# Optimization experiments

Hardware: AMD Instinct MI355X
Metric: run time of the kernel (lower is better)

## Reference

```python
import jax, jax.numpy as jnp
import numpy as np

N_SRC0, N_DST0 = 200000, 50000
N_DST1 = 10000
D_IN, D_HID = 128, 128


def _sage_mean(h, src, dst, n_dst, W_self, b_self, W_neigh, b_neigh, act):
    # gather messages from src nodes, mean-aggregate per dst node
    msg = h[src]                                             # [E, D]
    agg = jax.ops.segment_sum(msg, dst, num_segments=n_dst)  # [n_dst, D]
    deg = jax.ops.segment_sum(jnp.ones(dst.shape, h.dtype), dst, num_segments=n_dst)
    h_neigh = agg / jnp.maximum(deg, 1.0)[:, None]
    # DGL block convention: dst nodes are the first n_dst src nodes
    rst = h[:n_dst] @ W_self + b_self + h_neigh @ W_neigh + b_neigh
    return jax.nn.relu(rst) if act else rst


def setup_inputs() -> dict:
    key = jax.random.key(0)
    ks = jax.random.split(key, 12)
    s = 1.0 / np.sqrt(D_HID)
    return {
        "features": jax.random.normal(ks[0], (N_SRC0, D_IN), jnp.float32),
        "src0": jax.random.randint(ks[1], (800000,), 0, N_SRC0),
        "dst0": jax.random.randint(ks[2], (800000,), 0, N_DST0),
        "src1": jax.random.randint(ks[3], (160000,), 0, N_DST0),
        "dst1": jax.random.randint(ks[4], (160000,), 0, N_DST1),
        "W_init": jax.random.uniform(ks[5], (D_IN, D_HID), jnp.float32, -s, s),
        "b_init": jax.random.uniform(ks[6], (D_HID,), jnp.float32, -s, s),
        "W_self": jax.random.uniform(ks[7], (D_HID, D_HID), jnp.float32, -s, s),
        "b_self": jax.random.uniform(ks[8], (D_HID,), jnp.float32, -s, s),
        "W_neigh": jax.random.uniform(ks[9], (D_HID, D_HID), jnp.float32, -s, s),
        "b_neigh": jax.random.uniform(ks[10], (D_HID,), jnp.float32, -s, s),
    }


def reference(features, src0, dst0, src1, dst1, W_init, b_init, W_self, b_self, W_neigh, b_neigh):
    # fc_init + activation
    h = jax.nn.relu(features @ W_init + b_init)              # [N_SRC0, D_HID]
    # block 0 (act_flag True), dropout p=0.0 is identity
    h = _sage_mean(h, src0, dst0, N_DST0, W_self, b_self, W_neigh, b_neigh, act=True)
    # block 1 (last block: act_flag False)
    h = _sage_mean(h, src1, dst1, N_DST1, W_self, b_self, W_neigh, b_neigh, act=False)
    return jnp.squeeze(h, axis=1) if h.shape[1] == 1 else h  # h.squeeze(1) no-op for D_HID>1
```

## Files before the change

### kernel.cpp

```cpp
#include <hip/hip_runtime.h>
#include <stdint.h>
#include <stddef.h>


#define DIM 128
constexpr int N_SRC0 = 200000;
constexpr int N_DST0 = 50000;
constexpr int N_DST1 = 10000;
constexpr int E0 = 800000;
constexpr int E1 = 160000;
constexpr int MAXDEG = 64;

typedef __attribute__((ext_vector_type(8))) short bf16x8;
typedef __attribute__((ext_vector_type(4))) float f32x4;

__device__ __forceinline__ uint16_t f2bf(float f) {
  union { float f; uint32_t u; } v; v.f = f;
  return (uint16_t)((v.u + 0x7FFFu + ((v.u >> 16) & 1u)) >> 16);
}
__device__ __forceinline__ float bf2f(uint16_t h) {
  union { uint32_t u; float f; } v; v.u = ((uint32_t)h) << 16;
  return v.f;
}

__global__ __launch_bounds__(512) void prep_w_kernel(
    const float* __restrict__ W0, const float* __restrict__ W1,
    const float* __restrict__ W2, uint16_t* __restrict__ Wf,
    int* __restrict__ cnt, int ncnt) {
  int gid = blockIdx.x * 512 + threadIdx.x;
  if (gid < 3 * 16384) {
    int m = gid >> 14, idx = gid & 16383;
    const float* W = m == 0 ? W0 : (m == 1 ? W1 : W2);
    int j = idx & 7, lane = (idx >> 3) & 63, nt = (idx >> 9) & 7, kc = idx >> 12;
    int k = kc * 32 + (lane >> 4) * 8 + j;
    int n = nt * 16 + (lane & 15);
    Wf[gid] = f2bf(W[k * DIM + n]);
  }
  int z = gid - 3 * 16384;
  if (z >= 0 && z < ncnt) cnt[z] = 0;
}

__global__ __launch_bounds__(256) void place_kernel(
    const int* __restrict__ src0, const int* __restrict__ dst0,
    const int* __restrict__ src1, const int* __restrict__ dst1,
    int* __restrict__ cnt0, int* __restrict__ cnt1,
    int* __restrict__ eslot0, int* __restrict__ eslot1) {
  int part = blockIdx.x & 7;
  int bpp  = gridDim.x >> 3;
  int bidx = blockIdx.x >> 3;
  const int4* s04 = (const int4*)src0;
  const int4* d04 = (const int4*)dst0;
  const int4* s14 = (const int4*)src1;
  const int4* d14 = (const int4*)dst1;

  int lo = part * (N_DST0 / 8), hi = lo + (N_DST0 / 8);
  for (int i = bidx * 256 + threadIdx.x; i < E0 / 4; i += bpp * 256) {
    int4 d = d04[i]; int4 s = s04[i];
    if (d.x >= lo && d.x < hi) { int p = atomicAdd(&cnt0[d.x], 1); if (p < MAXDEG) eslot0[(size_t)d.x * MAXDEG + p] = s.x; }
    if (d.y >= lo && d.y < hi) { int p = atomicAdd(&cnt0[d.y], 1); if (p < MAXDEG) eslot0[(size_t)d.y * MAXDEG + p] = s.y; }
    if (d.z >= lo && d.z < hi) { int p = atomicAdd(&cnt0[d.z], 1); if (p < MAXDEG) eslot0[(size_t)d.z * MAXDEG + p] = s.z; }
    if (d.w >= lo && d.w < hi) { int p = atomicAdd(&cnt0[d.w], 1); if (p < MAXDEG) eslot0[(size_t)d.w * MAXDEG + p] = s.w; }
  }
  int lo1 = part * (N_DST1 / 8), hi1 = lo1 + (N_DST1 / 8);
  for (int i = bidx * 256 + threadIdx.x; i < E1 / 4; i += bpp * 256) {
    int4 d = d14[i]; int4 s = s14[i];
    if (d.x >= lo1 && d.x < hi1) { int p = atomicAdd(&cnt1[d.x], 1); if (p < MAXDEG) eslot1[(size_t)d.x * MAXDEG + p] = s.x; }
    if (d.y >= lo1 && d.y < hi1) { int p = atomicAdd(&cnt1[d.y], 1); if (p < MAXDEG) eslot1[(size_t)d.y * MAXDEG + p] = s.y; }
    if (d.z >= lo1 && d.z < hi1) { int p = atomicAdd(&cnt1[d.z], 1); if (p < MAXDEG) eslot1[(size_t)d.z * MAXDEG + p] = s.z; }
    if (d.w >= lo1 && d.w < hi1) { int p = atomicAdd(&cnt1[d.w], 1); if (p < MAXDEG) eslot1[(size_t)d.w * MAXDEG + p] = s.w; }
  }
}

__global__ __launch_bounds__(256) void fc_init_kernel(
    const float* __restrict__ feat, const uint16_t* __restrict__ Wf,
    const float* __restrict__ bias, uint16_t* __restrict__ hout) {
  __shared__ uint16_t wl[16384];
  __shared__ __align__(16) float tile[2][4096];
  {
    const uint4* g = (const uint4*)Wf;
    uint4* s = (uint4*)wl;
    for (int i = threadIdx.x; i < 2048; i += 256) s[i] = g[i];
  }
  const int tid = threadIdx.x;
  const int w = tid >> 6, lane = tid & 63;
  const int q = lane >> 4, m16 = lane & 15;
  const int sl = w >> 1, nh = w & 1;

  float bv[4];
#pragma unroll
  for (int j = 0; j < 4; j++) bv[j] = bias[(nh * 4 + j) * 16 + m16];

  const int ntiles = N_SRC0 / 32;
  const int stride = gridDim.x;

  auto stage = [&](int t, int buf) {
    const float* gbase = feat + (size_t)t * 4096 + w * 1024 + lane * 4;
    float* lbase = &tile[buf][w * 1024];
#pragma unroll
    for (int i = 0; i < 4; i++) {
      __builtin_amdgcn_global_load_lds(
          (const __attribute__((address_space(1))) uint32_t*)(gbase + i * 256),
          (__attribute__((address_space(3))) uint32_t*)(lbase + i * 256),
          16, 0, 0);
    }
  };

  int t = blockIdx.x;
  int cur = 0;
  if (t < ntiles) stage(t, 0);
  __syncthreads();

  while (t < ntiles) {
    int tn = t + stride;
    if (tn < ntiles) stage(tn, cur ^ 1);

    f32x4 acc[4];
#pragma unroll
    for (int j = 0; j < 4; j++) acc[j] = (f32x4){0.f, 0.f, 0.f, 0.f};

    const float* arow = &tile[cur][(sl * 16 + m16) * 128];
#pragma unroll
    for (int kc = 0; kc < 4; kc++) {
      float4 x0 = *(const float4*)(arow + kc * 32 + q * 8);
      float4 x1 = *(const float4*)(arow + kc * 32 + q * 8 + 4);
      float xs[8] = {x0.x, x0.y, x0.z, x0.w, x1.x, x1.y, x1.z, x1.w};
      bf16x8 a;
#pragma unroll
      for (int j = 0; j < 8; j++) a[j] = (short)f2bf(xs[j]);
#pragma unroll
      for (int j = 0; j < 4; j++) {
        int nt = nh * 4 + j;
        bf16x8 wv = *(const bf16x8*)&wl[((kc * 8 + nt) * 64 + lane) * 8];
        acc[j] = __builtin_amdgcn_mfma_f32_16x16x32_bf16(a, wv, acc[j], 0, 0, 0);
      }
    }

    int rowb = t * 32 + sl * 16 + q * 4;
#pragma unroll
    for (int j = 0; j < 4; j++)
#pragma unroll
      for (int r = 0; r < 4; r++) {
        float v = fmaxf(acc[j][r] + bv[j], 0.f);
        hout[(size_t)(rowb + r) * DIM + (nh * 4 + j) * 16 + m16] = f2bf(v);
      }

    __syncthreads();
    cur ^= 1;
    t = tn;
  }
}

__global__ __launch_bounds__(256) void agg_kernel(
    const int* __restrict__ eslot, const int* __restrict__ deg,
    const uint16_t* __restrict__ hsrc, uint16_t* __restrict__ hout, int n_dst) {
  int d = (blockIdx.x * 256 + threadIdx.x) >> 6;
  int lane = threadIdx.x & 63;
  if (d >= n_dst) return;
  const int* sl = eslot + (size_t)d * MAXDEG;
  int dg = deg[d];
  int dgc = dg < MAXDEG ? dg : MAXDEG;
  float a0 = 0.f, a1 = 0.f;
  int e = 0;
  for (; e + 4 <= dgc; e += 4) {
    int s0 = sl[e], s1 = sl[e + 1], s2 = sl[e + 2], s3 = sl[e + 3];
    uint32_t p0 = *(const uint32_t*)(hsrc + (size_t)s0 * DIM + lane * 2);
    uint32_t p1 = *(const uint32_t*)(hsrc + (size_t)s1 * DIM + lane * 2);
    uint32_t p2 = *(const uint32_t*)(hsrc + (size_t)s2 * DIM + lane * 2);
    uint32_t p3 = *(const uint32_t*)(hsrc + (size_t)s3 * DIM + lane * 2);
    a0 += bf2f((uint16_t)p0) + bf2f((uint16_t)p1) + bf2f((uint16_t)p2) + bf2f((uint16_t)p3);
    a1 += bf2f((uint16_t)(p0 >> 16)) + bf2f((uint16_t)(p1 >> 16)) +
          bf2f((uint16_t)(p2 >> 16)) + bf2f((uint16_t)(p3 >> 16));
  }
  for (; e < dgc; e++) {
    uint32_t p = *(const uint32_t*)(hsrc + (size_t)sl[e] * DIM + lane * 2);
    a0 += bf2f((uint16_t)p);
    a1 += bf2f((uint16_t)(p >> 16));
  }
  float inv = 1.f / fmaxf((float)dg, 1.f);
  uint32_t o = (uint32_t)f2bf(a0 * inv) | ((uint32_t)f2bf(a1 * inv) << 16);
  *(uint32_t*)(hout + (size_t)d * DIM + lane * 2) = o;
}

template <bool ACT, bool OUT_BF16>
__global__ __launch_bounds__(256) void sage_kernel(
    const uint16_t* __restrict__ hself, const uint16_t* __restrict__ hneigh,
    const uint16_t* __restrict__ WfS, const uint16_t* __restrict__ WfN,
    const float* __restrict__ bS, const float* __restrict__ bN,
    void* __restrict__ outp, int n_dst) {
  __shared__ uint16_t wS[16384];
  __shared__ uint16_t wN[16384];
  {
    const uint4* gS = (const uint4*)WfS;
    const uint4* gN = (const uint4*)WfN;
    uint4* sS = (uint4*)wS;
    uint4* sN = (uint4*)wN;
    for (int i = threadIdx.x; i < 2048; i += 256) { sS[i] = gS[i]; sN[i] = gN[i]; }
  }
  __syncthreads();

  int wave = (blockIdx.x * 256 + threadIdx.x) >> 6;
  int nwaves = (gridDim.x * 256) >> 6;
  int lane = threadIdx.x & 63;
  int q = lane >> 4, m16 = lane & 15;

  float bv[8];
#pragma unroll
  for (int nt = 0; nt < 8; nt++)
    bv[nt] = bS[nt * 16 + m16] + bN[nt * 16 + m16];

  const int nstrips = n_dst / 16;
  int s = wave;
  bf16x8 XS[4], XN[4];
  if (s < nstrips) {
    size_t ro = (size_t)(s * 16 + m16) * DIM + q * 8;
#pragma unroll
    for (int kc = 0; kc < 4; kc++) {
      XS[kc] = *(const bf16x8*)(hself + ro + kc * 32);
      XN[kc] = *(const bf16x8*)(hneigh + ro + kc * 32);
    }
  }

  while (s < nstrips) {
    int sn = s + nwaves;
    bf16x8 YS[4], YN[4];
    if (sn < nstrips) {
      size_t ro = (size_t)(sn * 16 + m16) * DIM + q * 8;
#pragma unroll
      for (int kc = 0; kc < 4; kc++) {
        YS[kc] = *(const bf16x8*)(hself + ro + kc * 32);
        YN[kc] = *(const bf16x8*)(hneigh + ro + kc * 32);
      }
    }

    f32x4 acc[8];
#pragma unroll
    for (int nt = 0; nt < 8; nt++) acc[nt] = (f32x4){0.f, 0.f, 0.f, 0.f};

#pragma unroll
    for (int kc = 0; kc < 4; kc++) {
#pragma unroll
      for (int nt = 0; nt < 8; nt++) {
        size_t fo = (size_t)((kc * 8 + nt) * 64 + lane) * 8;
        bf16x8 ws = *(const bf16x8*)&wS[fo];
        bf16x8 wn = *(const bf16x8*)&wN[fo];
        acc[nt] = __builtin_amdgcn_mfma_f32_16x16x32_bf16(XS[kc], ws, acc[nt], 0, 0, 0);
        acc[nt] = __builtin_amdgcn_mfma_f32_16x16x32_bf16(XN[kc], wn, acc[nt], 0, 0, 0);
      }
    }

    int m0 = s * 16;
#pragma unroll
    for (int nt = 0; nt < 8; nt++)
#pragma unroll
      for (int r = 0; r < 4; r++) {
        float v = acc[nt][r] + bv[nt];
        if (ACT) v = fmaxf(v, 0.f);
        size_t o = (size_t)(m0 + q * 4 + r) * DIM + nt * 16 + m16;
        if (OUT_BF16) ((uint16_t*)outp)[o] = f2bf(v);
        else          ((float*)outp)[o] = v;
      }

#pragma unroll
    for (int i = 0; i < 4; i++) { XS[i] = YS[i]; XN[i] = YN[i]; }
    s = sn;
  }
}

extern "C" void kernel_launch(void* const* d_in, const int* in_sizes, int n_in,
                              void* d_out, int out_size, void* d_ws, size_t ws_size,
                              hipStream_t stream) {
  const float* feat   = (const float*)d_in[0];
  const int* src0     = (const int*)d_in[1];
  const int* dst0     = (const int*)d_in[2];
  const int* src1     = (const int*)d_in[3];
  const int* dst1     = (const int*)d_in[4];
  const float* W_init = (const float*)d_in[5];
  const float* b_init = (const float*)d_in[6];
  const float* W_self = (const float*)d_in[7];
  const float* b_self = (const float*)d_in[8];
  const float* W_neigh= (const float*)d_in[9];
  const float* b_neigh= (const float*)d_in[10];

  char* ws = (char*)d_ws;
  uint16_t* h     = (uint16_t*)(ws + 0);
  uint16_t* h1    = (uint16_t*)(ws + 51200000);
  uint16_t* hn    = (uint16_t*)(ws + 64000000);
  int*      cnt0  = (int*)(ws + 76800000);
  int*      cnt1  = (int*)(ws + 77000000);
  int*      eslot0= (int*)(ws + 77040000);
  int*      eslot1= (int*)(ws + 89840000);
  uint16_t* WfI   = (uint16_t*)(ws + 92400000);
  uint16_t* WfS   = WfI + 16384;
  uint16_t* WfN   = WfS + 16384;

  prep_w_kernel<<<214, 512, 0, stream>>>(W_init, W_self, W_neigh, WfI, cnt0, 60000);
  place_kernel<<<1024, 256, 0, stream>>>(src0, dst0, src1, dst1,
                                         cnt0, cnt1, eslot0, eslot1);

  fc_init_kernel<<<512, 256, 0, stream>>>(feat, WfI, b_init, h);

  agg_kernel<<<N_DST0 / 4, 256, 0, stream>>>(eslot0, cnt0, h, hn, N_DST0);
  sage_kernel<true, true><<<512, 256, 0, stream>>>(h, hn, WfS, WfN, b_self, b_neigh,
                                                   h1, N_DST0);

  agg_kernel<<<N_DST1 / 4, 256, 0, stream>>>(eslot1, cnt1, h1, hn, N_DST1);
  sage_kernel<false, false><<<160, 256, 0, stream>>>(h1, hn, WfS, WfN, b_self, b_neigh,
                                                     d_out, N_DST1);
}
```

Measured before the change: 303.2 us.

## Fuse edge placement with fc_init, keep weights in registers, widen aggregation loads

Merges the edge-bucketing kernel and the fc_init GEMM into one launch, with even blocks doing atomic placement and odd blocks doing the GEMM so the two run concurrently. The GEMM now holds its weight fragments in registers instead of LDS and uses an XOR-swizzled LDS tile layout to cut bank conflicts. The aggregation kernel switches from 4-byte per-lane gathers to 16-byte loads, with four edges processed in parallel per wavefront and a cross-lane shuffle reduction at the end. The costs are higher register pressure and a mixed-role grid that could load-balance unevenly.

```diff
diff --git a/kernel.cpp b/kernel.cpp
--- a/kernel.cpp
+++ b/kernel.cpp
@@ -10,6 +10,9 @@
 constexpr int E0 = 800000;
 constexpr int E1 = 160000;
 constexpr int MAXDEG = 64;
+
+constexpr int FC_BLOCKS = 1024;
+constexpr int PLACE_BLOCKS = 1024;
 
 typedef __attribute__((ext_vector_type(8))) short bf16x8;
 typedef __attribute__((ext_vector_type(4))) float f32x4;
@@ -40,99 +43,107 @@
   if (z >= 0 && z < ncnt) cnt[z] = 0;
 }
 
-__global__ __launch_bounds__(256) void place_kernel(
+__global__ __launch_bounds__(256, 4) void place_fc_kernel(
     const int* __restrict__ src0, const int* __restrict__ dst0,
     const int* __restrict__ src1, const int* __restrict__ dst1,
     int* __restrict__ cnt0, int* __restrict__ cnt1,
-    int* __restrict__ eslot0, int* __restrict__ eslot1) {
-  int part = blockIdx.x & 7;
-  int bpp  = gridDim.x >> 3;
-  int bidx = blockIdx.x >> 3;
-  const int4* s04 = (const int4*)src0;
-  const int4* d04 = (const int4*)dst0;
-  const int4* s14 = (const int4*)src1;
-  const int4* d14 = (const int4*)dst1;
-
-  int lo = part * (N_DST0 / 8), hi = lo + (N_DST0 / 8);
-  for (int i = bidx * 256 + threadIdx.x; i < E0 / 4; i += bpp * 256) {
-    int4 d = d04[i]; int4 s = s04[i];
-    if (d.x >= lo && d.x < hi) { int p = atomicAdd(&cnt0[d.x], 1); if (p < MAXDEG) eslot0[(size_t)d.x * MAXDEG + p] = s.x; }
-    if (d.y >= lo && d.y < hi) { int p = atomicAdd(&cnt0[d.y], 1); if (p < MAXDEG) eslot0[(size_t)d.y * MAXDEG + p] = s.y; }
-    if (d.z >= lo && d.z < hi) { int p = atomicAdd(&cnt0[d.z], 1); if (p < MAXDEG) eslot0[(size_t)d.z * MAXDEG + p] = s.z; }
-    if (d.w >= lo && d.w < hi) { int p = atomicAdd(&cnt0[d.w], 1); if (p < MAXDEG) eslot0[(size_t)d.w * MAXDEG + p] = s.w; }
-  }
-  int lo1 = part * (N_DST1 / 8), hi1 = lo1 + (N_DST1 / 8);
-  for (int i = bidx * 256 + threadIdx.x; i < E1 / 4; i += bpp * 256) {
-    int4 d = d14[i]; int4 s = s14[i];
-    if (d.x >= lo1 && d.x < hi1) { int p = atomicAdd(&cnt1[d.x], 1); if (p < MAXDEG) eslot1[(size_t)d.x * MAXDEG + p] = s.x; }
-    if (d.y >= lo1 && d.y < hi1) { int p = atomicAdd(&cnt1[d.y], 1); if (p < MAXDEG) eslot1[(size_t)d.y * MAXDEG + p] = s.y; }
-    if (d.z >= lo1 && d.z < hi1) { int p = atomicAdd(&cnt1[d.z], 1); if (p < MAXDEG) eslot1[(size_t)d.z * MAXDEG + p] = s.z; }
-    if (d.w >= lo1 && d.w < hi1) { int p = atomicAdd(&cnt1[d.w], 1); if (p < MAXDEG) eslot1[(size_t)d.w * MAXDEG + p] = s.w; }
-  }
-}
-
-__global__ __launch_bounds__(256) void fc_init_kernel(
+    int* __restrict__ eslot0, int* __restrict__ eslot1,
     const float* __restrict__ feat, const uint16_t* __restrict__ Wf,
     const float* __restrict__ bias, uint16_t* __restrict__ hout) {
-  __shared__ uint16_t wl[16384];
   __shared__ __align__(16) float tile[2][4096];
-  {
-    const uint4* g = (const uint4*)Wf;
-    uint4* s = (uint4*)wl;
-    for (int i = threadIdx.x; i < 2048; i += 256) s[i] = g[i];
-  }
+
+  if ((blockIdx.x & 1) == 0) {
+    int pb = blockIdx.x >> 1;
+    int part = pb & 7;
+    int bpp  = PLACE_BLOCKS >> 3;
+    int bidx = pb >> 3;
+    const int4* s04 = (const int4*)src0;
+    const int4* d04 = (const int4*)dst0;
+    const int4* s14 = (const int4*)src1;
+    const int4* d14 = (const int4*)dst1;
+
+    int lo = part * (N_DST0 / 8), hi = lo + (N_DST0 / 8);
+    for (int i = bidx * 256 + threadIdx.x; i < E0 / 4; i += bpp * 256) {
+      int4 d = d04[i]; int4 s = s04[i];
+      if (d.x >= lo && d.x < hi) { int p = atomicAdd(&cnt0[d.x], 1); if (p < MAXDEG) eslot0[(size_t)d.x * MAXDEG + p] = s.x; }
+      if (d.y >= lo && d.y < hi) { int p = atomicAdd(&cnt0[d.y], 1); if (p < MAXDEG) eslot0[(size_t)d.y * MAXDEG + p] = s.y; }
+      if (d.z >= lo && d.z < hi) { int p = atomicAdd(&cnt0[d.z], 1); if (p < MAXDEG) eslot0[(size_t)d.z * MAXDEG + p] = s.z; }
+      if (d.w >= lo && d.w < hi) { int p = atomicAdd(&cnt0[d.w], 1); if (p < MAXDEG) eslot0[(size_t)d.w * MAXDEG + p] = s.w; }
+    }
+    int lo1 = part * (N_DST1 / 8), hi1 = lo1 + (N_DST1 / 8);
+    for (int i = bidx * 256 + threadIdx.x; i < E1 / 4; i += bpp * 256) {
+      int4 d = d14[i]; int4 s = s14[i];
+      if (d.x >= lo1 && d.x < hi1) { int p = atomicAdd(&cnt1[d.x], 1); if (p < MAXDEG) eslot1[(size_t)d.x * MAXDEG + p] = s.x; }
+      if (d.y >= lo1 && d.y < hi1) { int p = atomicAdd(&cnt1[d.y], 1); if (p < MAXDEG) eslot1[(size_t)d.y * MAXDEG + p] = s.y; }
+      if (d.z >= lo1 && d.z < hi1) { int p = atomicAdd(&cnt1[d.z], 1); if (p < MAXDEG) eslot1[(size_t)d.z * MAXDEG + p] = s.z; }
+      if (d.w >= lo1 && d.w < hi1) { int p = atomicAdd(&cnt1[d.w], 1); if (p < MAXDEG) eslot1[(size_t)d.w * MAXDEG + p] = s.w; }
+    }
+    return;
+  }
+
   const int tid = threadIdx.x;
   const int w = tid >> 6, lane = tid & 63;
   const int q = lane >> 4, m16 = lane & 15;
   const int sl = w >> 1, nh = w & 1;
 
+  bf16x8 wv[4][4];
+#pragma unroll
+  for (int kc = 0; kc < 4; kc++)
+#pragma unroll
+    for (int j = 0; j < 4; j++)
+      wv[kc][j] = *(const bf16x8*)&Wf[((size_t)((kc * 8 + nh * 4 + j) * 64 + lane)) * 8];
+
   float bv[4];
 #pragma unroll
   for (int j = 0; j < 4; j++) bv[j] = bias[(nh * 4 + j) * 16 + m16];
 
   const int ntiles = N_SRC0 / 32;
-  const int stride = gridDim.x;
-
+
+  const int lrow0 = w * 8 + (lane >> 5);
   auto stage = [&](int t, int buf) {
-    const float* gbase = feat + (size_t)t * 4096 + w * 1024 + lane * 4;
-    float* lbase = &tile[buf][w * 1024];
 #pragma unroll
     for (int i = 0; i < 4; i++) {
+      int row = lrow0 + i * 2;
+      int g = (lane & 31) ^ (row & 7);
+      const float* gs = feat + (size_t)t * 4096 + row * 128 + g * 4;
+      float* ld = &tile[buf][w * 1024 + i * 256];
       __builtin_amdgcn_global_load_lds(
-          (const __attribute__((address_space(1))) uint32_t*)(gbase + i * 256),
-          (__attribute__((address_space(3))) uint32_t*)(lbase + i * 256),
+          (const __attribute__((address_space(1))) uint32_t*)gs,
+          (__attribute__((address_space(3))) uint32_t*)ld,
           16, 0, 0);
     }
   };
 
-  int t = blockIdx.x;
+  int t = blockIdx.x >> 1;
   int cur = 0;
   if (t < ntiles) stage(t, 0);
   __syncthreads();
 
+  const int trow = sl * 16 + m16;
+  const int sw = trow & 7;
+
   while (t < ntiles) {
-    int tn = t + stride;
+    int tn = t + FC_BLOCKS;
     if (tn < ntiles) stage(tn, cur ^ 1);
 
     f32x4 acc[4];
 #pragma unroll
     for (int j = 0; j < 4; j++) acc[j] = (f32x4){0.f, 0.f, 0.f, 0.f};
 
-    const float* arow = &tile[cur][(sl * 16 + m16) * 128];
+    const char* rb = (const char*)&tile[cur][0] + trow * 512;
 #pragma unroll
     for (int kc = 0; kc < 4; kc++) {
-      float4 x0 = *(const float4*)(arow + kc * 32 + q * 8);
-      float4 x1 = *(const float4*)(arow + kc * 32 + q * 8 + 4);
-      float xs[8] = {x0.x, x0.y, x0.z, x0.w, x1.x, x1.y, x1.z, x1.w};
+      int g0 = kc * 8 + q * 2;
+      float4 x0 = *(const float4*)(rb + ((g0    ) ^ sw) * 16);
+      float4 x1 = *(const float4*)(rb + ((g0 + 1) ^ sw) * 16);
       bf16x8 a;
-#pragma unroll
-      for (int j = 0; j < 8; j++) a[j] = (short)f2bf(xs[j]);
-#pragma unroll
-      for (int j = 0; j < 4; j++) {
-        int nt = nh * 4 + j;
-        bf16x8 wv = *(const bf16x8*)&wl[((kc * 8 + nt) * 64 + lane) * 8];
-        acc[j] = __builtin_amdgcn_mfma_f32_16x16x32_bf16(a, wv, acc[j], 0, 0, 0);
-      }
+      a[0] = (short)f2bf(x0.x); a[1] = (short)f2bf(x0.y);
+      a[2] = (short)f2bf(x0.z); a[3] = (short)f2bf(x0.w);
+      a[4] = (short)f2bf(x1.x); a[5] = (short)f2bf(x1.y);
+      a[6] = (short)f2bf(x1.z); a[7] = (short)f2bf(x1.w);
+#pragma unroll
+      for (int j = 0; j < 4; j++)
+        acc[j] = __builtin_amdgcn_mfma_f32_16x16x32_bf16(a, wv[kc][j], acc[j], 0, 0, 0);
     }
 
     int rowb = t * 32 + sl * 16 + q * 4;
@@ -159,26 +170,57 @@
   const int* sl = eslot + (size_t)d * MAXDEG;
   int dg = deg[d];
   int dgc = dg < MAXDEG ? dg : MAXDEG;
-  float a0 = 0.f, a1 = 0.f;
+  int qr = lane >> 4;
+  int c  = lane & 15;
+
+  float a0 = 0.f, a1 = 0.f, a2 = 0.f, a3 = 0.f;
+  float a4 = 0.f, a5 = 0.f, a6 = 0.f, a7 = 0.f;
+
+#define ACC4(P)                                                          \
+  a0 += bf2f((uint16_t)(P).x); a1 += bf2f((uint16_t)((P).x >> 16));      \
+  a2 += bf2f((uint16_t)(P).y); a3 += bf2f((uint16_t)((P).y >> 16));      \
+  a4 += bf2f((uint16_t)(P).z); a5 += bf2f((uint16_t)((P).z >> 16));      \
+  a6 += bf2f((uint16_t)(P).w); a7 += bf2f((uint16_t)((P).w >> 16));
+
   int e = 0;
+  for (; e + 8 <= dgc; e += 8) {
+    int s0 = sl[e + qr];
+    int s1 = sl[e + 4 + qr];
+    uint4 p0 = *(const uint4*)(hsrc + (size_t)s0 * DIM + c * 8);
+    uint4 p1 = *(const uint4*)(hsrc + (size_t)s1 * DIM + c * 8);
+    ACC4(p0); ACC4(p1);
+  }
   for (; e + 4 <= dgc; e += 4) {
-    int s0 = sl[e], s1 = sl[e + 1], s2 = sl[e + 2], s3 = sl[e + 3];
-    uint32_t p0 = *(const uint32_t*)(hsrc + (size_t)s0 * DIM + lane * 2);
-    uint32_t p1 = *(const uint32_t*)(hsrc + (size_t)s1 * DIM + lane * 2);
-    uint32_t p2 = *(const uint32_t*)(hsrc + (size_t)s2 * DIM + lane * 2);
-    uint32_t p3 = *(const uint32_t*)(hsrc + (size_t)s3 * DIM + lane * 2);
-    a0 += bf2f((uint16_t)p0) + bf2f((uint16_t)p1) + bf2f((uint16_t)p2) + bf2f((uint16_t)p3);
-    a1 += bf2f((uint16_t)(p0 >> 16)) + bf2f((uint16_t)(p1 >> 16)) +
-          bf2f((uint16_t)(p2 >> 16)) + bf2f((uint16_t)(p3 >> 16));
-  }
-  for (; e < dgc; e++) {
-    uint32_t p = *(const uint32_t*)(hsrc + (size_t)sl[e] * DIM + lane * 2);
-    a0 += bf2f((uint16_t)p);
-    a1 += bf2f((uint16_t)(p >> 16));
-  }
-  float inv = 1.f / fmaxf((float)dg, 1.f);
-  uint32_t o = (uint32_t)f2bf(a0 * inv) | ((uint32_t)f2bf(a1 * inv) << 16);
-  *(uint32_t*)(hout + (size_t)d * DIM + lane * 2) = o;
+    int s0 = sl[e + qr];
+    uint4 p0 = *(const uint4*)(hsrc + (size_t)s0 * DIM + c * 8);
+    ACC4(p0);
+  }
+  int rem = dgc - e;
+  if (qr < rem) {
+    int s0 = sl[e + qr];
+    uint4 p0 = *(const uint4*)(hsrc + (size_t)s0 * DIM + c * 8);
+    ACC4(p0);
+  }
+#undef ACC4
+
+  a0 += __shfl_xor(a0, 16); a0 += __shfl_xor(a0, 32);
+  a1 += __shfl_xor(a1, 16); a1 += __shfl_xor(a1, 32);
+  a2 += __shfl_xor(a2, 16); a2 += __shfl_xor(a2, 32);
+  a3 += __shfl_xor(a3, 16); a3 += __shfl_xor(a3, 32);
+  a4 += __shfl_xor(a4, 16); a4 += __shfl_xor(a4, 32);
+  a5 += __shfl_xor(a5, 16); a5 += __shfl_xor(a5, 32);
+  a6 += __shfl_xor(a6, 16); a6 += __shfl_xor(a6, 32);
+  a7 += __shfl_xor(a7, 16); a7 += __shfl_xor(a7, 32);
+
+  if (qr == 0) {
+    float inv = 1.f / fmaxf((float)dg, 1.f);
+    uint4 o;
+    o.x = (uint32_t)f2bf(a0 * inv) | ((uint32_t)f2bf(a1 * inv) << 16);
+    o.y = (uint32_t)f2bf(a2 * inv) | ((uint32_t)f2bf(a3 * inv) << 16);
+    o.z = (uint32_t)f2bf(a4 * inv) | ((uint32_t)f2bf(a5 * inv) << 16);
+    o.w = (uint32_t)f2bf(a6 * inv) | ((uint32_t)f2bf(a7 * inv) << 16);
+    *(uint4*)(hout + (size_t)d * DIM + c * 8) = o;
+  }
 }
 
 template <bool ACT, bool OUT_BF16>
@@ -294,10 +336,10 @@
   uint16_t* WfN   = WfS + 16384;
 
   prep_w_kernel<<<214, 512, 0, stream>>>(W_init, W_self, W_neigh, WfI, cnt0, 60000);
-  place_kernel<<<1024, 256, 0, stream>>>(src0, dst0, src1, dst1,
-                                         cnt0, cnt1, eslot0, eslot1);
-
-  fc_init_kernel<<<512, 256, 0, stream>>>(feat, WfI, b_init, h);
+
+  place_fc_kernel<<<PLACE_BLOCKS + FC_BLOCKS, 256, 0, stream>>>(
+      src0, dst0, src1, dst1, cnt0, cnt1, eslot0, eslot1,
+      feat, WfI, b_init, h);
 
   agg_kernel<<<N_DST0 / 4, 256, 0, stream>>>(eslot0, cnt0, h, hn, N_DST0);
   sage_kernel<true, true><<<512, 256, 0, stream>>>(h, hn, WfS, WfN, b_self, b_neigh,
```

Result: faster. 270.6 us (-10.8%).
